# Kernel optimization log

Measured on AMD Instinct MI355X. Metric: run time of the kernel, lower is better.

The kernel has to match this reference:

```python
import jax, jax.numpy as jnp
import numpy as np

B, H, S, D = 4, 16, 2048, 64

def setup_inputs() -> dict:
    key = jax.random.key(0)
    k1, k2, k3 = jax.random.split(key, 3)
    x1 = jax.random.normal(k1, (B, H, S, D), dtype=jnp.float32)
    x2 = jax.random.normal(k2, (B, H, S, D), dtype=jnp.float32)
    x3 = jax.random.normal(k3, (B, H, S, D), dtype=jnp.float32)
    scale = jnp.float32(1.0 / np.sqrt(D))  # 0.125
    return {"x1": x1, "x2": x2, "x3": x3, "scale": scale}

def reference(x1, x2, x3, scale):
    # scores: [B, H, S, S] = Q @ K^T * scale
    scores = jnp.einsum('bhqd,bhkd->bhqk', x1, x2) * scale
    att = jax.nn.softmax(scores, axis=-1)
    # out: [B, H, S, D] = att @ V
    return jnp.einsum('bhqk,bhkd->bhqd', att, x3)
```

## Files before the change

kernel.cpp:

```cpp
#include <hip/hip_runtime.h>
#include <hip/hip_bf16.h>

typedef __attribute__((ext_vector_type(8))) short short8;
typedef __attribute__((ext_vector_type(16))) float f32x16;
typedef __attribute__((ext_vector_type(4))) float f32x4;
typedef __attribute__((ext_vector_type(2))) unsigned uint2v;

#define S_LEN 2048
#define D_DIM 64
#define QT 256
#define KT 64
#define NT (S_LEN / KT)
#define SMAXC 16.0f
#define SWZ(r) ((((r) & 7) ^ (((r) >> 3) & 7)) << 4)

static __device__ __forceinline__ unsigned cvt_pk(float lo, float hi) {
  unsigned r;
  asm("v_cvt_pk_bf16_f32 %0, %1, %2" : "=v"(r) : "v"(lo), "v"(hi));
  return r;
}

static __device__ __forceinline__ void plswap(unsigned &a, unsigned &b) {
  uint2v r = __builtin_amdgcn_permlane32_swap(a, b, false, false);
  a = r.x; b = r.y;
}

union U8 { unsigned u[4]; short8 s; };

__global__ __attribute__((amdgpu_flat_work_group_size(512, 512),
                          amdgpu_waves_per_eu(4, 4)))
void attn_fwd(const float* __restrict__ Qg, const float* __restrict__ Kg,
              const float* __restrict__ Vg, const float* __restrict__ sp,
              float* __restrict__ Og)
{
  __shared__ __align__(16) char smem[36864];

  const int tid = threadIdx.x;
  const int w   = tid >> 6;
  const int l   = tid & 63;
  const int q32 = l & 31;
  const int hi  = l >> 5;

  const int wg   = blockIdx.x;
  const int xcd  = wg & 7;
  const int slot = wg >> 3;
  const int bh   = xcd * 8 + (slot >> 3);
  const int qb   = (slot & 7) * QT;

  const float* Qh = Qg + (size_t)bh * (S_LEN * D_DIM);
  const float* Kh = Kg + (size_t)bh * (S_LEN * D_DIM);
  const float* Vh = Vg + (size_t)bh * (S_LEN * D_DIM);
  float*       Oh = Og + (size_t)bh * (S_LEN * D_DIM);

  const float qscale = sp[0] * 1.4426950408889634f;

  short8 qf[4];
  {
    const float* qrow = Qh + (size_t)(qb + w * 32 + q32) * D_DIM + hi * 8;
#pragma unroll
    for (int dk = 0; dk < 4; ++dk) {
      float4 f0 = *(const float4*)(qrow + dk * 16);
      float4 f1 = *(const float4*)(qrow + dk * 16 + 4);
      U8 u;
      u.u[0] = cvt_pk(f0.x * qscale, f0.y * qscale);
      u.u[1] = cvt_pk(f0.z * qscale, f0.w * qscale);
      u.u[2] = cvt_pk(f1.x * qscale, f1.y * qscale);
      u.u[3] = cvt_pk(f1.z * qscale, f1.w * qscale);
      qf[dk] = u.s;
    }
  }

  f32x16 o0, o1;
#pragma unroll
  for (int r = 0; r < 16; ++r) { o0[r] = 0.f; o1[r] = 0.f; }
  f32x4 lacc;
  lacc[0] = 0.f; lacc[1] = 0.f; lacc[2] = 0.f; lacc[3] = 0.f;

  const int krow = tid >> 3, kcolf = (tid & 7) * 8;
  const int vdd  = (tid & 15) * 4, vkk = (tid >> 4) * 2;
  const int kd   = (krow << 7) + ((kcolf * 2) ^ SWZ(krow));
  const int vdo0 = 8192 + ((vdd + 0) << 7) + ((vkk * 2) ^ SWZ(vdd + 0));
  const int vdo1 = 8192 + ((vdd + 1) << 7) + ((vkk * 2) ^ SWZ(vdd + 1));
  const int vdo2 = 8192 + ((vdd + 2) << 7) + ((vkk * 2) ^ SWZ(vdd + 2));
  const int vdo3 = 8192 + ((vdd + 3) << 7) + ((vkk * 2) ^ SWZ(vdd + 3));

  const int swzA = SWZ(q32);
  const int swzB = swzA ^ 64;
  const int kq   = (q32 << 7);

  const float* kptr = Kh + (size_t)krow * D_DIM + kcolf;
  const float* vptr = Vh + (size_t)vkk * D_DIM + vdd;

  unsigned kH[4], vH[4];
  {
    float4 a = ((const float4*)kptr)[0], b = ((const float4*)kptr)[1];
    kH[0] = cvt_pk(a.x, a.y); kH[1] = cvt_pk(a.z, a.w);
    kH[2] = cvt_pk(b.x, b.y); kH[3] = cvt_pk(b.z, b.w);
    float4 r0 = *(const float4*)(vptr);
    float4 r1 = *(const float4*)(vptr + D_DIM);
    vH[0] = cvt_pk(r0.x, r1.x);
    vH[1] = cvt_pk(r0.y, r1.y);
    vH[2] = cvt_pk(r0.z, r1.z);
    vH[3] = cvt_pk(r0.w, r1.w);
  }

  for (int t = 0; t < NT; ++t) {
    const int buf = (t & 1) * 16384;
    const bool more = (t + 1 < NT);
    float4 pa, pb, va, vbq;
    if (more) {
      const float* ks = kptr + (size_t)(t + 1) * (KT * D_DIM);
      const float* vs = vptr + (size_t)(t + 1) * (KT * D_DIM);
      pa  = ((const float4*)ks)[0];
      pb  = ((const float4*)ks)[1];
      va  = *(const float4*)(vs);
      vbq = *(const float4*)(vs + D_DIM);
    }

    *(uint4*)(smem + buf + kd) = make_uint4(kH[0], kH[1], kH[2], kH[3]);
    *(unsigned*)(smem + buf + vdo0) = vH[0];
    *(unsigned*)(smem + buf + vdo1) = vH[1];
    *(unsigned*)(smem + buf + vdo2) = vH[2];
    *(unsigned*)(smem + buf + vdo3) = vH[3];
    __syncthreads();

#pragma unroll
    for (int sb = 0; sb < 2; ++sb) {
      const int kbo  = buf + kq + (sb ? (32 << 7) : 0);
      const int swzK = sb ? swzB : swzA;
      f32x16 st;
#pragma unroll
      for (int r = 0; r < 16; ++r) st[r] = -SMAXC;
      __builtin_amdgcn_s_setprio(1);
#pragma unroll
      for (int dk = 0; dk < 4; ++dk) {
        short8 ka = *(const short8*)(smem + kbo + ((dk * 32 + hi * 16) ^ swzK));
        st = __builtin_amdgcn_mfma_f32_32x32x16_bf16(ka, qf[dk], st, 0, 0, 0);
      }
      __builtin_amdgcn_s_setprio(0);

#pragma unroll
      for (int r = 0; r < 16; ++r)
        st[r] = __builtin_amdgcn_exp2f(st[r]);
#pragma unroll
      for (int j = 0; j < 4; ++j)
        lacc[j] += (st[j] + st[j + 4]) + (st[j + 8] + st[j + 12]);

      unsigned pk[8];
#pragma unroll
      for (int j = 0; j < 8; ++j) pk[j] = cvt_pk(st[2 * j], st[2 * j + 1]);
      plswap(pk[0], pk[2]);
      plswap(pk[1], pk[3]);
      plswap(pk[4], pk[6]);
      plswap(pk[5], pk[7]);
      U8 f0, f1;
      f0.u[0] = pk[0]; f0.u[1] = pk[1]; f0.u[2] = pk[2]; f0.u[3] = pk[3];
      f1.u[0] = pk[4]; f1.u[1] = pk[5]; f1.u[2] = pk[6]; f1.u[3] = pk[7];

      __builtin_amdgcn_s_setprio(1);
      {
        const int vb0 = buf + 8192 + kq;
        const int vb1 = vb0 + (32 << 7);
        short8 x0 = *(const short8*)(smem + vb0 + ((sb * 64 + 0  + hi * 16) ^ swzA));
        short8 x1 = *(const short8*)(smem + vb0 + ((sb * 64 + 32 + hi * 16) ^ swzA));
        o0 = __builtin_amdgcn_mfma_f32_32x32x16_bf16(x0, f0.s, o0, 0, 0, 0);
        o0 = __builtin_amdgcn_mfma_f32_32x32x16_bf16(x1, f1.s, o0, 0, 0, 0);
        short8 y0 = *(const short8*)(smem + vb1 + ((sb * 64 + 0  + hi * 16) ^ swzB));
        short8 y1 = *(const short8*)(smem + vb1 + ((sb * 64 + 32 + hi * 16) ^ swzB));
        o1 = __builtin_amdgcn_mfma_f32_32x32x16_bf16(y0, f0.s, o1, 0, 0, 0);
        o1 = __builtin_amdgcn_mfma_f32_32x32x16_bf16(y1, f1.s, o1, 0, 0, 0);
      }
      __builtin_amdgcn_s_setprio(0);
    }

    if (more) {
      kH[0] = cvt_pk(pa.x, pa.y); kH[1] = cvt_pk(pa.z, pa.w);
      kH[2] = cvt_pk(pb.x, pb.y); kH[3] = cvt_pk(pb.z, pb.w);
      vH[0] = cvt_pk(va.x, vbq.x);
      vH[1] = cvt_pk(va.y, vbq.y);
      vH[2] = cvt_pk(va.z, vbq.z);
      vH[3] = cvt_pk(va.w, vbq.w);
    }
  }

  float l_run = (lacc[0] + lacc[1]) + (lacc[2] + lacc[3]);
  float l_tot = l_run + __shfl_xor(l_run, 32, 64);
  float rl = 1.0f / l_tot;
  float* Ow = (float*)smem + w * (32 * 36);
#pragma unroll
  for (int nb = 0; nb < 2; ++nb) {
    __syncthreads();
#pragma unroll
    for (int rr = 0; rr < 4; ++rr) {
      float4 v;
      if (nb == 0) { v.x = o0[rr*4+0]*rl; v.y = o0[rr*4+1]*rl; v.z = o0[rr*4+2]*rl; v.w = o0[rr*4+3]*rl; }
      else         { v.x = o1[rr*4+0]*rl; v.y = o1[rr*4+1]*rl; v.z = o1[rr*4+2]*rl; v.w = o1[rr*4+3]*rl; }
      *(float4*)&Ow[q32 * 36 + rr * 8 + hi * 4] = v;
    }
    __syncthreads();
#pragma unroll
    for (int i = 0; i < 4; ++i) {
      int e = i * 256 + l * 4;
      int row = e >> 5, col = e & 31;
      float4 v = *(const float4*)&Ow[row * 36 + col];
      *(float4*)(Oh + (size_t)(qb + w * 32 + row) * D_DIM + nb * 32 + col) = v;
    }
  }
}

extern "C" void kernel_launch(void* const* d_in, const int* in_sizes, int n_in,
                              void* d_out, int out_size, void* d_ws, size_t ws_size,
                              hipStream_t stream) {
  (void)in_sizes; (void)n_in; (void)d_ws; (void)ws_size; (void)out_size;
  const float* Q  = (const float*)d_in[0];
  const float* K  = (const float*)d_in[1];
  const float* V  = (const float*)d_in[2];
  const float* sp = (const float*)d_in[3];
  float* O = (float*)d_out;
  dim3 grid((S_LEN / QT) * 64);
  attn_fwd<<<grid, 512, 0, stream>>>(Q, K, V, sp, O);
}
```

Baseline: 103.8 us.

## Switch attention inner loop to 16x16x32 MFMA and single-barrier double buffering

Replaces the 32x32x16 MFMA tiling with 16x16x32 bf16 MFMAs, splitting each wave's 32 queries into two 16-row sub-tiles and reshuffling P with permlane32 and permlane16 swaps. The K/V staging now writes the next tile into the alternate buffer between the two halves of compute, leaving one barrier per iteration. It also adds an s_sleep stagger for half the workgroups so their memory phases are offset. The aim is better MFMA/exp interleaving and less barrier stall, at the cost of more instructions, more MFMA issues and changed register pressure.

```diff
diff --git a/kernel.cpp b/kernel.cpp
--- a/kernel.cpp
+++ b/kernel.cpp
@@ -2,9 +2,9 @@
 #include <hip/hip_bf16.h>
 
 typedef __attribute__((ext_vector_type(8))) short short8;
-typedef __attribute__((ext_vector_type(16))) float f32x16;
 typedef __attribute__((ext_vector_type(4))) float f32x4;
 typedef __attribute__((ext_vector_type(2))) unsigned uint2v;
+typedef unsigned long long ull;
 
 #define S_LEN 2048
 #define D_DIM 64
@@ -25,7 +25,13 @@
   a = r.x; b = r.y;
 }
 
+static __device__ __forceinline__ void pl16swap(unsigned &a, unsigned &b) {
+  asm volatile("v_permlane16_swap_b32 %0, %1" : "+v"(a), "+v"(b));
+}
+
 union U8 { unsigned u[4]; short8 s; };
+
+#define MFMA16(A, B, C) __builtin_amdgcn_mfma_f32_16x16x32_bf16((A), (B), (C), 0, 0, 0)
 
 __global__ __attribute__((amdgpu_flat_work_group_size(512, 512),
                           amdgpu_waves_per_eu(4, 4)))
@@ -33,13 +39,13 @@
               const float* __restrict__ Vg, const float* __restrict__ sp,
               float* __restrict__ Og)
 {
-  __shared__ __align__(16) char smem[36864];
+  __shared__ __align__(16) char smem[32768];
 
   const int tid = threadIdx.x;
-  const int w   = tid >> 6;
+  const int wid = tid >> 6;
   const int l   = tid & 63;
-  const int q32 = l & 31;
-  const int hi  = l >> 5;
+  const int q16 = l & 15;
+  const int h   = (l >> 4) & 3;
 
   const int wg   = blockIdx.x;
   const int xcd  = wg & 7;
@@ -47,6 +53,10 @@
   const int bh   = xcd * 8 + (slot >> 3);
   const int qb   = (slot & 7) * QT;
 
+  if ((slot ^ (slot >> 5)) & 1) {
+    __builtin_amdgcn_s_sleep(48);
+  }
+
   const float* Qh = Qg + (size_t)bh * (S_LEN * D_DIM);
   const float* Kh = Kg + (size_t)bh * (S_LEN * D_DIM);
   const float* Vh = Vg + (size_t)bh * (S_LEN * D_DIM);
@@ -54,156 +64,195 @@
 
   const float qscale = sp[0] * 1.4426950408889634f;
 
-  short8 qf[4];
-  {
-    const float* qrow = Qh + (size_t)(qb + w * 32 + q32) * D_DIM + hi * 8;
-#pragma unroll
-    for (int dk = 0; dk < 4; ++dk) {
-      float4 f0 = *(const float4*)(qrow + dk * 16);
-      float4 f1 = *(const float4*)(qrow + dk * 16 + 4);
+  short8 qfA[2], qfB[2];
+#pragma unroll
+  for (int qs = 0; qs < 2; ++qs) {
+    const float* qrow = Qh + (size_t)(qb + wid * 32 + qs * 16 + q16) * D_DIM + h * 8;
+#pragma unroll
+    for (int ks = 0; ks < 2; ++ks) {
+      float4 f0 = *(const float4*)(qrow + ks * 32);
+      float4 f1 = *(const float4*)(qrow + ks * 32 + 4);
       U8 u;
       u.u[0] = cvt_pk(f0.x * qscale, f0.y * qscale);
       u.u[1] = cvt_pk(f0.z * qscale, f0.w * qscale);
       u.u[2] = cvt_pk(f1.x * qscale, f1.y * qscale);
       u.u[3] = cvt_pk(f1.z * qscale, f1.w * qscale);
-      qf[dk] = u.s;
-    }
-  }
-
-  f32x16 o0, o1;
-#pragma unroll
-  for (int r = 0; r < 16; ++r) { o0[r] = 0.f; o1[r] = 0.f; }
-  f32x4 lacc;
-  lacc[0] = 0.f; lacc[1] = 0.f; lacc[2] = 0.f; lacc[3] = 0.f;
-
-  const int krow = tid >> 3, kcolf = (tid & 7) * 8;
+      if (qs == 0) qfA[ks] = u.s; else qfB[ks] = u.s;
+    }
+  }
+
+  f32x4 oa0, oa1, oa2, oa3, ob0, ob1, ob2, ob3;
+#pragma unroll
+  for (int r = 0; r < 4; ++r) {
+    oa0[r] = 0.f; oa1[r] = 0.f; oa2[r] = 0.f; oa3[r] = 0.f;
+    ob0[r] = 0.f; ob1[r] = 0.f; ob2[r] = 0.f; ob3[r] = 0.f;
+  }
+  float l_a = 0.f, l_b = 0.f;
+
+  int rbase[4], rswz[4];
+#pragma unroll
+  for (int f = 0; f < 4; ++f) {
+    rbase[f] = (f * 16 + q16) << 7;
+    rswz[f]  = SWZ(f * 16 + q16);
+  }
+
+  const int krow = tid >> 3, kc = tid & 7;
+  const int kd0  = (krow << 7) + ((kc * 16) ^ SWZ(krow));
   const int vdd  = (tid & 15) * 4, vkk = (tid >> 4) * 2;
-  const int kd   = (krow << 7) + ((kcolf * 2) ^ SWZ(krow));
   const int vdo0 = 8192 + ((vdd + 0) << 7) + ((vkk * 2) ^ SWZ(vdd + 0));
   const int vdo1 = 8192 + ((vdd + 1) << 7) + ((vkk * 2) ^ SWZ(vdd + 1));
   const int vdo2 = 8192 + ((vdd + 2) << 7) + ((vkk * 2) ^ SWZ(vdd + 2));
   const int vdo3 = 8192 + ((vdd + 3) << 7) + ((vkk * 2) ^ SWZ(vdd + 3));
 
-  const int swzA = SWZ(q32);
-  const int swzB = swzA ^ 64;
-  const int kq   = (q32 << 7);
-
-  const float* kptr = Kh + (size_t)krow * D_DIM + kcolf;
+  const float* kptr = Kh + (size_t)krow * D_DIM + kc * 8;
   const float* vptr = Vh + (size_t)vkk * D_DIM + vdd;
 
-  unsigned kH[4], vH[4];
   {
     float4 a = ((const float4*)kptr)[0], b = ((const float4*)kptr)[1];
-    kH[0] = cvt_pk(a.x, a.y); kH[1] = cvt_pk(a.z, a.w);
-    kH[2] = cvt_pk(b.x, b.y); kH[3] = cvt_pk(b.z, b.w);
+    *(uint4*)(smem + kd0) = make_uint4(cvt_pk(a.x, a.y), cvt_pk(a.z, a.w),
+                                       cvt_pk(b.x, b.y), cvt_pk(b.z, b.w));
     float4 r0 = *(const float4*)(vptr);
     float4 r1 = *(const float4*)(vptr + D_DIM);
-    vH[0] = cvt_pk(r0.x, r1.x);
-    vH[1] = cvt_pk(r0.y, r1.y);
-    vH[2] = cvt_pk(r0.z, r1.z);
-    vH[3] = cvt_pk(r0.w, r1.w);
-  }
+    *(unsigned*)(smem + vdo0) = cvt_pk(r0.x, r1.x);
+    *(unsigned*)(smem + vdo1) = cvt_pk(r0.y, r1.y);
+    *(unsigned*)(smem + vdo2) = cvt_pk(r0.z, r1.z);
+    *(unsigned*)(smem + vdo3) = cvt_pk(r0.w, r1.w);
+  }
+  __syncthreads();
 
   for (int t = 0; t < NT; ++t) {
-    const int buf = (t & 1) * 16384;
+    const int buf  = (t & 1) * 16384;
+    const int bufw = buf ^ 16384;
     const bool more = (t + 1 < NT);
-    float4 pa, pb, va, vbq;
+
+    float4 pa, pb, v0, v1;
     if (more) {
       const float* ks = kptr + (size_t)(t + 1) * (KT * D_DIM);
       const float* vs = vptr + (size_t)(t + 1) * (KT * D_DIM);
-      pa  = ((const float4*)ks)[0];
-      pb  = ((const float4*)ks)[1];
-      va  = *(const float4*)(vs);
-      vbq = *(const float4*)(vs + D_DIM);
-    }
-
-    *(uint4*)(smem + buf + kd) = make_uint4(kH[0], kH[1], kH[2], kH[3]);
-    *(unsigned*)(smem + buf + vdo0) = vH[0];
-    *(unsigned*)(smem + buf + vdo1) = vH[1];
-    *(unsigned*)(smem + buf + vdo2) = vH[2];
-    *(unsigned*)(smem + buf + vdo3) = vH[3];
+      pa = ((const float4*)ks)[0]; pb = ((const float4*)ks)[1];
+      v0 = *(const float4*)(vs);
+      v1 = *(const float4*)(vs + D_DIM);
+    }
+
+#define HALF(bb)                                                               \
+    {                                                                          \
+      f32x4 s00, s01, s10, s11;                                                \
+      _Pragma("unroll")                                                        \
+      for (int r = 0; r < 4; ++r) { s00[r] = -SMAXC; s01[r] = -SMAXC;          \
+                                    s10[r] = -SMAXC; s11[r] = -SMAXC; }        \
+      __builtin_amdgcn_s_setprio(1);                                           \
+      {                                                                        \
+        short8 k00 = *(const short8*)(smem + buf + rbase[2*(bb)+0] +           \
+                      ((0 * 64 + h * 16) ^ rswz[2*(bb)+0]));                   \
+        s00 = MFMA16(k00, qfA[0], s00); s10 = MFMA16(k00, qfB[0], s10);        \
+        short8 k10 = *(const short8*)(smem + buf + rbase[2*(bb)+1] +           \
+                      ((0 * 64 + h * 16) ^ rswz[2*(bb)+1]));                   \
+        s01 = MFMA16(k10, qfA[0], s01); s11 = MFMA16(k10, qfB[0], s11);        \
+        short8 k01 = *(const short8*)(smem + buf + rbase[2*(bb)+0] +           \
+                      ((1 * 64 + h * 16) ^ rswz[2*(bb)+0]));                   \
+        s00 = MFMA16(k01, qfA[1], s00); s10 = MFMA16(k01, qfB[1], s10);        \
+        short8 k11 = *(const short8*)(smem + buf + rbase[2*(bb)+1] +           \
+                      ((1 * 64 + h * 16) ^ rswz[2*(bb)+1]));                   \
+        s01 = MFMA16(k11, qfA[1], s01); s11 = MFMA16(k11, qfB[1], s11);        \
+      }                                                                        \
+      __builtin_amdgcn_s_setprio(0);                                           \
+      U8 fA, fB;                                                               \
+      {                                                                        \
+        _Pragma("unroll")                                                      \
+        for (int r = 0; r < 4; ++r) {                                          \
+          s00[r] = __builtin_amdgcn_exp2f(s00[r]);                             \
+          s01[r] = __builtin_amdgcn_exp2f(s01[r]);                             \
+        }                                                                      \
+        l_a += ((s00[0] + s00[1]) + (s00[2] + s00[3]))                         \
+             + ((s01[0] + s01[1]) + (s01[2] + s01[3]));                        \
+        unsigned wE0 = cvt_pk(s00[0], s00[1]), wE1 = cvt_pk(s00[2], s00[3]);   \
+        unsigned wO0 = cvt_pk(s01[0], s01[1]), wO1 = cvt_pk(s01[2], s01[3]);   \
+        plswap(wE0, wO0); pl16swap(wE0, wO0);                                  \
+        plswap(wE1, wO1); pl16swap(wE1, wO1);                                  \
+        fA.u[0] = wE0; fA.u[1] = wE1; fA.u[2] = wO0; fA.u[3] = wO1;            \
+      }                                                                        \
+      {                                                                        \
+        _Pragma("unroll")                                                      \
+        for (int r = 0; r < 4; ++r) {                                          \
+          s10[r] = __builtin_amdgcn_exp2f(s10[r]);                             \
+          s11[r] = __builtin_amdgcn_exp2f(s11[r]);                             \
+        }                                                                      \
+        l_b += ((s10[0] + s10[1]) + (s10[2] + s10[3]))                         \
+             + ((s11[0] + s11[1]) + (s11[2] + s11[3]));                        \
+        unsigned wE0 = cvt_pk(s10[0], s10[1]), wE1 = cvt_pk(s10[2], s10[3]);   \
+        unsigned wO0 = cvt_pk(s11[0], s11[1]), wO1 = cvt_pk(s11[2], s11[3]);   \
+        plswap(wE0, wO0); pl16swap(wE0, wO0);                                  \
+        plswap(wE1, wO1); pl16swap(wE1, wO1);                                  \
+        fB.u[0] = wE0; fB.u[1] = wE1; fB.u[2] = wO0; fB.u[3] = wO1;            \
+      }                                                                        \
+      __builtin_amdgcn_s_setprio(1);                                           \
+      {                                                                        \
+        short8 va0 = *(const short8*)(smem + buf + 8192 + rbase[0] +           \
+                      (((bb) * 64 + h * 16) ^ rswz[0]));                       \
+        oa0 = MFMA16(va0, fA.s, oa0); ob0 = MFMA16(va0, fB.s, ob0);            \
+        short8 va1 = *(const short8*)(smem + buf + 8192 + rbase[1] +           \
+                      (((bb) * 64 + h * 16) ^ rswz[1]));                       \
+        oa1 = MFMA16(va1, fA.s, oa1); ob1 = MFMA16(va1, fB.s, ob1);            \
+        short8 va2 = *(const short8*)(smem + buf + 8192 + rbase[2] +           \
+                      (((bb) * 64 + h * 16) ^ rswz[2]));                       \
+        oa2 = MFMA16(va2, fA.s, oa2); ob2 = MFMA16(va2, fB.s, ob2);            \
+        short8 va3 = *(const short8*)(smem + buf + 8192 + rbase[3] +           \
+                      (((bb) * 64 + h * 16) ^ rswz[3]));                       \
+        oa3 = MFMA16(va3, fA.s, oa3); ob3 = MFMA16(va3, fB.s, ob3);            \
+      }                                                                        \
+      __builtin_amdgcn_s_setprio(0);                                           \
+    }
+
+    HALF(0)
+
+    if (more) {
+      *(uint4*)(smem + bufw + kd0) =
+          make_uint4(cvt_pk(pa.x, pa.y), cvt_pk(pa.z, pa.w),
+                     cvt_pk(pb.x, pb.y), cvt_pk(pb.z, pb.w));
+    }
+
+    HALF(1)
+#undef HALF
+
+    if (more) {
+      *(unsigned*)(smem + bufw + vdo0) = cvt_pk(v0.x, v1.x);
+      *(unsigned*)(smem + bufw + vdo1) = cvt_pk(v0.y, v1.y);
+      *(unsigned*)(smem + bufw + vdo2) = cvt_pk(v0.z, v1.z);
+      *(unsigned*)(smem + bufw + vdo3) = cvt_pk(v0.w, v1.w);
+    }
     __syncthreads();
-
-#pragma unroll
-    for (int sb = 0; sb < 2; ++sb) {
-      const int kbo  = buf + kq + (sb ? (32 << 7) : 0);
-      const int swzK = sb ? swzB : swzA;
-      f32x16 st;
-#pragma unroll
-      for (int r = 0; r < 16; ++r) st[r] = -SMAXC;
-      __builtin_amdgcn_s_setprio(1);
-#pragma unroll
-      for (int dk = 0; dk < 4; ++dk) {
-        short8 ka = *(const short8*)(smem + kbo + ((dk * 32 + hi * 16) ^ swzK));
-        st = __builtin_amdgcn_mfma_f32_32x32x16_bf16(ka, qf[dk], st, 0, 0, 0);
+  }
+
+  float la = l_a + __shfl_xor(l_a, 16, 64); la += __shfl_xor(la, 32, 64);
+  float lb = l_b + __shfl_xor(l_b, 16, 64); lb += __shfl_xor(lb, 32, 64);
+  const float rla = 1.0f / la;
+  const float rlb = 1.0f / lb;
+  float* Ow = (float*)smem + wid * (16 * 40);
+#pragma unroll
+  for (int qs = 0; qs < 2; ++qs) {
+    const float rl = qs ? rlb : rla;
+    const int rowbase = qb + wid * 32 + qs * 16;
+#pragma unroll
+    for (int nb = 0; nb < 2; ++nb) {
+      __syncthreads();
+#pragma unroll
+      for (int dl = 0; dl < 2; ++dl) {
+        const int dblk = nb * 2 + dl;
+        f32x4 p;
+        if (qs == 0) p = (dblk == 0) ? oa0 : (dblk == 1) ? oa1 : (dblk == 2) ? oa2 : oa3;
+        else         p = (dblk == 0) ? ob0 : (dblk == 1) ? ob1 : (dblk == 2) ? ob2 : ob3;
+        float4 v; v.x = p[0] * rl; v.y = p[1] * rl; v.z = p[2] * rl; v.w = p[3] * rl;
+        *(float4*)&Ow[q16 * 40 + dl * 16 + h * 4] = v;
       }
-      __builtin_amdgcn_s_setprio(0);
-
-#pragma unroll
-      for (int r = 0; r < 16; ++r)
-        st[r] = __builtin_amdgcn_exp2f(st[r]);
-#pragma unroll
-      for (int j = 0; j < 4; ++j)
-        lacc[j] += (st[j] + st[j + 4]) + (st[j + 8] + st[j + 12]);
-
-      unsigned pk[8];
-#pragma unroll
-      for (int j = 0; j < 8; ++j) pk[j] = cvt_pk(st[2 * j], st[2 * j + 1]);
-      plswap(pk[0], pk[2]);
-      plswap(pk[1], pk[3]);
-      plswap(pk[4], pk[6]);
-      plswap(pk[5], pk[7]);
-      U8 f0, f1;
-      f0.u[0] = pk[0]; f0.u[1] = pk[1]; f0.u[2] = pk[2]; f0.u[3] = pk[3];
-      f1.u[0] = pk[4]; f1.u[1] = pk[5]; f1.u[2] = pk[6]; f1.u[3] = pk[7];
-
-      __builtin_amdgcn_s_setprio(1);
+      __syncthreads();
       {
-        const int vb0 = buf + 8192 + kq;
-        const int vb1 = vb0 + (32 << 7);
-        short8 x0 = *(const short8*)(smem + vb0 + ((sb * 64 + 0  + hi * 16) ^ swzA));
-        short8 x1 = *(const short8*)(smem + vb0 + ((sb * 64 + 32 + hi * 16) ^ swzA));
-        o0 = __builtin_amdgcn_mfma_f32_32x32x16_bf16(x0, f0.s, o0, 0, 0, 0);
-        o0 = __builtin_amdgcn_mfma_f32_32x32x16_bf16(x1, f1.s, o0, 0, 0, 0);
-        short8 y0 = *(const short8*)(smem + vb1 + ((sb * 64 + 0  + hi * 16) ^ swzB));
-        short8 y1 = *(const short8*)(smem + vb1 + ((sb * 64 + 32 + hi * 16) ^ swzB));
-        o1 = __builtin_amdgcn_mfma_f32_32x32x16_bf16(y0, f0.s, o1, 0, 0, 0);
-        o1 = __builtin_amdgcn_mfma_f32_32x32x16_bf16(y1, f1.s, o1, 0, 0, 0);
+        const int row = l >> 2, cb = (l & 3) * 8;
+        float4 x = *(const float4*)&Ow[row * 40 + cb];
+        float4 y = *(const float4*)&Ow[row * 40 + cb + 4];
+        float* dst = Oh + (size_t)(rowbase + row) * D_DIM + nb * 32 + cb;
+        *(float4*)dst = x;
+        *(float4*)(dst + 4) = y;
       }
-      __builtin_amdgcn_s_setprio(0);
-    }
-
-    if (more) {
-      kH[0] = cvt_pk(pa.x, pa.y); kH[1] = cvt_pk(pa.z, pa.w);
-      kH[2] = cvt_pk(pb.x, pb.y); kH[3] = cvt_pk(pb.z, pb.w);
-      vH[0] = cvt_pk(va.x, vbq.x);
-      vH[1] = cvt_pk(va.y, vbq.y);
-      vH[2] = cvt_pk(va.z, vbq.z);
-      vH[3] = cvt_pk(va.w, vbq.w);
-    }
-  }
-
-  float l_run = (lacc[0] + lacc[1]) + (lacc[2] + lacc[3]);
-  float l_tot = l_run + __shfl_xor(l_run, 32, 64);
-  float rl = 1.0f / l_tot;
-  float* Ow = (float*)smem + w * (32 * 36);
-#pragma unroll
-  for (int nb = 0; nb < 2; ++nb) {
-    __syncthreads();
-#pragma unroll
-    for (int rr = 0; rr < 4; ++rr) {
-      float4 v;
-      if (nb == 0) { v.x = o0[rr*4+0]*rl; v.y = o0[rr*4+1]*rl; v.z = o0[rr*4+2]*rl; v.w = o0[rr*4+3]*rl; }
-      else         { v.x = o1[rr*4+0]*rl; v.y = o1[rr*4+1]*rl; v.z = o1[rr*4+2]*rl; v.w = o1[rr*4+3]*rl; }
-      *(float4*)&Ow[q32 * 36 + rr * 8 + hi * 4] = v;
-    }
-    __syncthreads();
-#pragma unroll
-    for (int i = 0; i < 4; ++i) {
-      int e = i * 256 + l * 4;
-      int row = e >> 5, col = e & 31;
-      float4 v = *(const float4*)&Ow[row * 36 + col];
-      *(float4*)(Oh + (size_t)(qb + w * 32 + row) * D_DIM + nb * 32 + col) = v;
     }
   }
 }
```

New measurement: 92.30 us. -11.1%, faster.
